# Kernel tuning notes

Hardware: AMD Instinct MI355X
Metric: run time of the kernel (lower is better)

## Reference

```python
import jax, jax.numpy as jnp
import numpy as np

B, H, S, D = 2, 16, 2048, 128


def setup_inputs() -> dict:
    key = jax.random.key(0)
    ks = jax.random.split(key, 11)
    s = 1.0 / np.sqrt(D)
    return {
        "query": jax.random.normal(ks[0], (B, H, S, D), dtype=jnp.float32),
        "key": jax.random.normal(ks[1], (B, H, S, D), dtype=jnp.float32),
        "value": jax.random.normal(ks[2], (B, H, S, D), dtype=jnp.float32),
        "Wq": jax.random.normal(ks[3], (D, D), dtype=jnp.float32) * s,
        "bq": jnp.zeros((D,), dtype=jnp.float32),
        "Wk": jax.random.normal(ks[4], (D, D), dtype=jnp.float32) * s,
        "bk": jnp.zeros((D,), dtype=jnp.float32),
        "Wv": jax.random.normal(ks[5], (D, D), dtype=jnp.float32) * s,
        "bv": jnp.zeros((D,), dtype=jnp.float32),
        "Wo": jax.random.normal(ks[6], (D, D), dtype=jnp.float32) * s,
        "bo": jnp.zeros((D,), dtype=jnp.float32),
    }


def reference(query, key, value, Wq, bq, Wk, bk, Wv, bv, Wo, bo):
    # Linear projections (torch Linear: x @ W^T + b) on last dim of [B,H,S,D]
    q = jnp.einsum("bhsd,ed->bhse", query, Wq) + bq
    k = jnp.einsum("bhsd,ed->bhse", key, Wk) + bk
    v = jnp.einsum("bhsd,ed->bhse", value, Wv) + bv
    scale = jnp.sqrt(jnp.asarray(D, dtype=q.dtype))
    q = q / scale
    qk = jnp.einsum("bhse,bhte->bhst", q, k)  # [B,H,S,S] scores
    attn = jax.nn.softmax(qk, axis=-1)
    # dropout_p = 0.0 -> identity
    out = jnp.einsum("bhst,bhtd->bhsd", attn, v)
    out = jnp.einsum("bhsd,ed->bhse", out, Wo) + bo
    return out
```

## Files before the change

### kernel.cpp

```cpp
#include <hip/hip_runtime.h>
#include <hip/hip_bf16.h>
#include <type_traits>
#include <math.h>

typedef __bf16 bf16x8 __attribute__((ext_vector_type(8)));
typedef float floatx4 __attribute__((ext_vector_type(4)));
typedef float floatx16 __attribute__((ext_vector_type(16)));

#define S_LEN 2048
#define D_DIM 128
#define NTOK (2 * 16 * 2048)
#define KVB 64
#define NKV (S_LEN / KVB)

template <typename TIN, typename TOUT>
__device__ __forceinline__ void proj_body4(
    const TIN* __restrict__ x, const float* __restrict__ W,
    const float* __restrict__ b, TOUT* __restrict__ y, float out_scale,
    int chunk0, __bf16 (*Wl)[128]) {
  const int tid = threadIdx.x;
  const int wave = tid >> 6, lane = tid & 63;
  const int g = lane >> 4, lr = lane & 15;

  for (int it = 0; it < 16; ++it) {
    int lin = it * 1024 + tid * 4;
    float4 w4 = *reinterpret_cast<const float4*>(W + lin);
    int r = lin >> 7, c = lin & 127;
    Wl[r][c]     = (__bf16)w4.x;
    Wl[r][c + 1] = (__bf16)w4.y;
    Wl[r][c + 2] = (__bf16)w4.z;
    Wl[r][c + 3] = (__bf16)w4.w;
  }
  __syncthreads();

  float be[8];
#pragma unroll
  for (int nt = 0; nt < 8; ++nt) be[nt] = b[nt * 16 + lr];

  for (int ch = 0; ch < 4; ++ch) {
    const int rbase = (chunk0 + ch) * 64;
    const int arow = rbase + wave * 16 + lr;

    floatx4 acc[8];
#pragma unroll
    for (int i = 0; i < 8; ++i) acc[i] = floatx4{0.f, 0.f, 0.f, 0.f};

#pragma unroll
    for (int kc = 0; kc < 4; ++kc) {
      bf16x8 af;
      const TIN* xp = x + (size_t)arow * D_DIM + kc * 32 + g * 8;
      if constexpr (std::is_same<TIN, float>::value) {
        float4 f0 = *reinterpret_cast<const float4*>(xp);
        float4 f1 = *reinterpret_cast<const float4*>(xp + 4);
        af[0] = (__bf16)f0.x; af[1] = (__bf16)f0.y;
        af[2] = (__bf16)f0.z; af[3] = (__bf16)f0.w;
        af[4] = (__bf16)f1.x; af[5] = (__bf16)f1.y;
        af[6] = (__bf16)f1.z; af[7] = (__bf16)f1.w;
      } else {
        af = *reinterpret_cast<const bf16x8*>(xp);
      }
#pragma unroll
      for (int nt = 0; nt < 8; ++nt) {
        bf16x8 wf = *reinterpret_cast<const bf16x8*>(&Wl[nt * 16 + lr][kc * 32 + g * 8]);
        acc[nt] = __builtin_amdgcn_mfma_f32_16x16x32_bf16(af, wf, acc[nt], 0, 0, 0);
      }
    }

#pragma unroll
    for (int nt = 0; nt < 8; ++nt) {
      int e = nt * 16 + lr;
#pragma unroll
      for (int j = 0; j < 4; ++j) {
        int row = rbase + wave * 16 + g * 4 + j;
        float val = (acc[nt][j] + be[nt]) * out_scale;
        y[(size_t)row * D_DIM + e] = (TOUT)val;
      }
    }
  }
}

__global__ __launch_bounds__(256) void qkv_proj_kernel(
    const float* __restrict__ xq, const float* __restrict__ xk,
    const float* __restrict__ xv, const float* __restrict__ Wq,
    const float* __restrict__ Wk, const float* __restrict__ Wv,
    const float* __restrict__ bq, const float* __restrict__ bk,
    const float* __restrict__ bv, __bf16* yq, __bf16* yk, __bf16* yv,
    float qscale) {
  __shared__ alignas(16) __bf16 Wl[128][128];
  const int which = blockIdx.y;
  const float* x = which == 0 ? xq : which == 1 ? xk : xv;
  const float* W = which == 0 ? Wq : which == 1 ? Wk : Wv;
  const float* b = which == 0 ? bq : which == 1 ? bk : bv;
  __bf16* y = which == 0 ? yq : which == 1 ? yk : yv;
  float sc = which == 0 ? qscale : 1.0f;
  proj_body4<float, __bf16>(x, W, b, y, sc, blockIdx.x * 4, Wl);
}

__global__ __launch_bounds__(256) void o_proj_kernel(
    const __bf16* __restrict__ x, const float* __restrict__ W,
    const float* __restrict__ b, float* __restrict__ y) {
  __shared__ alignas(16) __bf16 Wl[128][128];
  proj_body4<__bf16, float>(x, W, b, y, 1.0f, blockIdx.x * 4, Wl);
}

__device__ __forceinline__ unsigned swz(int row, unsigned byteoff) {
  return byteoff ^ (((unsigned)(row ^ (row >> 3)) & 7u) << 4);
}

__device__ __forceinline__ unsigned pack2(float lo, float hi) {
  union { __bf16 h[2]; unsigned u; } r;
  r.h[0] = (__bf16)lo; r.h[1] = (__bf16)hi;
  return r.u;
}

__global__ __launch_bounds__(256, 2) void attn_kernel(
    const __bf16* __restrict__ q, const __bf16* __restrict__ k,
    const __bf16* __restrict__ v, __bf16* __restrict__ o) {
  __shared__ alignas(16) unsigned char smem[65536];

  const int tid = threadIdx.x;
  const int wave = tid >> 6, lane = tid & 63;
  const int ql = lane & 31;
  const int h = lane >> 5;

  const int bh = blockIdx.x;
  const int qbase = blockIdx.y * 128;
  const __bf16* qp = q + (size_t)bh * S_LEN * D_DIM;
  const __bf16* kp = k + (size_t)bh * S_LEN * D_DIM;
  const __bf16* vp = v + (size_t)bh * S_LEN * D_DIM;
  __bf16* op = o + (size_t)bh * S_LEN * D_DIM;

  const int qrow = qbase + wave * 32 + ql;
  bf16x8 qf[8];
#pragma unroll
  for (int kc = 0; kc < 8; ++kc)
    qf[kc] = *reinterpret_cast<const bf16x8*>(
        qp + (size_t)qrow * D_DIM + kc * 16 + h * 8);

  floatx16 ot[4];
#pragma unroll
  for (int d = 0; d < 4; ++d)
#pragma unroll
    for (int r = 0; r < 16; ++r) ot[d][r] = 0.f;
  float m_r = -1e30f, l_r = 0.f;

  const int cc = tid & 15;
  const int pr4 = (tid >> 4) * 4;
  const int ce = cc * 8;

  unsigned Rk[4];
#pragma unroll
  for (int x = 0; x < 4; ++x)
    Rk[x] = (unsigned)(h * 1024) +
            (((unsigned)(ql * 16)) ^ ((unsigned)h << 4) ^ ((unsigned)x << 5));
  const unsigned Rv0 = 32768u + (unsigned)(h * 2048) +
                       (((unsigned)(ql * 16)) ^ (((unsigned)(ql >> 3)) << 4));
  const unsigned Rv1 = Rv0 ^ 64u;
  const unsigned kx = ((unsigned)(cc & 7)) << 4;
  unsigned Wk_[4];
#pragma unroll
  for (int j = 0; j < 4; ++j)
    Wk_[j] = ((unsigned)(cc * 1024 + (pr4 + j) * 16)) ^ kx;
  unsigned Wv_[8];
  {
    unsigned vbase = 32768u + (unsigned)((pr4 >> 3) * 2048 + ce * 16 + (pr4 & 7) * 2);
#pragma unroll
    for (int e = 0; e < 8; ++e)
      Wv_[e] = vbase | (((unsigned)e << 4) ^ kx);
  }

  {
    const __bf16* kr = kp + (size_t)pr4 * D_DIM + ce;
    const __bf16* vr = vp + (size_t)pr4 * D_DIM + ce;
    bf16x8 kR[4];
    union { bf16x8 v8; unsigned short s[8]; } vR[4];
#pragma unroll
    for (int j = 0; j < 4; ++j) {
      kR[j] = *reinterpret_cast<const bf16x8*>(kr + j * D_DIM);
      vR[j].v8 = *reinterpret_cast<const bf16x8*>(vr + j * D_DIM);
    }
#pragma unroll
    for (int j = 0; j < 4; ++j)
      *reinterpret_cast<bf16x8*>(smem + Wk_[j]) = kR[j];
#pragma unroll
    for (int e = 0; e < 8; ++e) {
      uint2 w;
      w.x = (unsigned)vR[0].s[e] | ((unsigned)vR[1].s[e] << 16);
      w.y = (unsigned)vR[2].s[e] | ((unsigned)vR[3].s[e] << 16);
      *reinterpret_cast<uint2*>(smem + Wv_[e]) = w;
    }
  }

  const __bf16* krp = kp + ((size_t)KVB + pr4) * D_DIM + ce;
  const __bf16* vrp = vp + ((size_t)KVB + pr4) * D_DIM + ce;

#pragma unroll 2
  for (int t = 0; t < NKV; ++t) {
    const unsigned cb = (unsigned)(t & 1) * 16384u;
    const bool hn = (t + 1 < NKV);

    __syncthreads();

    bf16x8 kR[4];
    union { bf16x8 v8; unsigned short s[8]; } vR[4];
    if (hn) {
#pragma unroll
      for (int j = 0; j < 4; ++j) {
        kR[j] = *reinterpret_cast<const bf16x8*>(krp + j * D_DIM);
        vR[j].v8 = *reinterpret_cast<const bf16x8*>(vrp + j * D_DIM);
      }
      krp += (size_t)KVB * D_DIM;
      vrp += (size_t)KVB * D_DIM;
    }

    floatx16 st[2];
#pragma unroll
    for (int kvh = 0; kvh < 2; ++kvh)
#pragma unroll
      for (int r = 0; r < 16; ++r) st[kvh][r] = 0.f;
    __builtin_amdgcn_s_setprio(1);
#pragma unroll
    for (int kc = 0; kc < 8; ++kc) {
      bf16x8 kf0 = *reinterpret_cast<const bf16x8*>(
          smem + cb + Rk[kc & 3] + (unsigned)(kc * 2048));
      bf16x8 kf1 = *reinterpret_cast<const bf16x8*>(
          smem + cb + Rk[kc & 3] + (unsigned)(kc * 2048 + 512));
      st[0] = __builtin_amdgcn_mfma_f32_32x32x16_bf16(kf0, qf[kc], st[0], 0, 0, 0);
      st[1] = __builtin_amdgcn_mfma_f32_32x32x16_bf16(kf1, qf[kc], st[1], 0, 0, 0);
    }
    __builtin_amdgcn_s_setprio(0);

    if (hn) {
      const unsigned nb = cb ^ 16384u;
#pragma unroll
      for (int j = 0; j < 4; ++j)
        *reinterpret_cast<bf16x8*>(smem + nb + Wk_[j]) = kR[j];
#pragma unroll
      for (int e = 0; e < 8; ++e) {
        uint2 w;
        w.x = (unsigned)vR[0].s[e] | ((unsigned)vR[1].s[e] << 16);
        w.y = (unsigned)vR[2].s[e] | ((unsigned)vR[3].s[e] << 16);
        *reinterpret_cast<uint2*>(smem + nb + Wv_[e]) = w;
      }
    }

    float t8[8];
#pragma unroll
    for (int i = 0; i < 8; ++i)
      t8[i] = fmaxf(fmaxf(st[0][i], st[0][i + 8]), fmaxf(st[1][i], st[1][i + 8]));
    float pmax = fmaxf(fmaxf(fmaxf(t8[0], t8[4]), fmaxf(t8[1], t8[5])),
                       fmaxf(fmaxf(t8[2], t8[6]), fmaxf(t8[3], t8[7])));
    pmax = fmaxf(pmax, __shfl_xor(pmax, 32));
    if (!__all(pmax - m_r <= 8.0f)) {
      float mnew = fmaxf(m_r, pmax);
      float sc_f = __builtin_amdgcn_exp2f(m_r - mnew);
      m_r = mnew;
      l_r *= sc_f;
#pragma unroll
      for (int d = 0; d < 4; ++d)
#pragma unroll
        for (int r = 0; r < 16; ++r) ot[d][r] *= sc_f;
    }
#pragma unroll
    for (int kvh = 0; kvh < 2; ++kvh)
#pragma unroll
      for (int r = 0; r < 16; ++r)
        st[kvh][r] = __builtin_amdgcn_exp2f(st[kvh][r] - m_r);
    float s8[8];
#pragma unroll
    for (int i = 0; i < 8; ++i)
      s8[i] = (st[0][i] + st[0][i + 8]) + (st[1][i] + st[1][i + 8]);
    float psum = ((s8[0] + s8[4]) + (s8[1] + s8[5])) +
                 ((s8[2] + s8[6]) + (s8[3] + s8[7]));
    psum += __shfl_xor(psum, 32);
    l_r += psum;

#pragma unroll
    for (int ks = 0; ks < 4; ++ks) {
      const int kvh = ks >> 1;
      const int r2a = (2 * ks) & 3;
      const int r2b = r2a + 1;
      unsigned ua0 = pack2(st[kvh][r2a * 4 + 0], st[kvh][r2a * 4 + 1]);
      unsigned ua1 = pack2(st[kvh][r2a * 4 + 2], st[kvh][r2a * 4 + 3]);
      unsigned ub0 = pack2(st[kvh][r2b * 4 + 0], st[kvh][r2b * 4 + 1]);
      unsigned ub1 = pack2(st[kvh][r2b * 4 + 2], st[kvh][r2b * 4 + 3]);
      union { unsigned u[4]; bf16x8 v8; } pw;
#if __has_builtin(__builtin_amdgcn_permlane32_swap)
      {
        auto r0 = __builtin_amdgcn_permlane32_swap(ua0, ub0, false, false);
        auto r1 = __builtin_amdgcn_permlane32_swap(ua1, ub1, false, false);
        pw.u[0] = r0[0];
        pw.u[1] = r1[0];
        pw.u[2] = r0[1];
        pw.u[3] = r1[1];
      }
#else
      {
        unsigned a0x = __shfl_xor(ua0, 32), a1x = __shfl_xor(ua1, 32);
        unsigned b0x = __shfl_xor(ub0, 32), b1x = __shfl_xor(ub1, 32);
        pw.u[0] = h ? b0x : ua0;
        pw.u[1] = h ? b1x : ua1;
        pw.u[2] = h ? ub0 : a0x;
        pw.u[3] = h ? ub1 : a1x;
      }
#endif
      __builtin_amdgcn_s_setprio(1);
#pragma unroll
      for (int db = 0; db < 4; ++db) {
        const unsigned base = (db & 1) ? Rv1 : Rv0;
        bf16x8 vf = *reinterpret_cast<const bf16x8*>(
            smem + cb + base + (unsigned)(ks * 4096 + db * 512));
        ot[db] = __builtin_amdgcn_mfma_f32_32x32x16_bf16(vf, pw.v8, ot[db], 0, 0, 0);
      }
      __builtin_amdgcn_s_setprio(0);
    }
  }

  __syncthreads();
  const float inv_l = 1.0f / l_r;
  const int qloc = wave * 32 + ql;
#pragma unroll
  for (int db = 0; db < 4; ++db)
#pragma unroll
    for (int r = 0; r < 16; ++r) {
      int d = db * 32 + (r & 3) + 8 * (r >> 2) + 4 * h;
      *reinterpret_cast<__bf16*>(smem + swz(qloc, qloc * 256u + d * 2u)) =
          (__bf16)(ot[db][r] * inv_l);
    }
  __syncthreads();
#pragma unroll
  for (int it = 0; it < 8; ++it) {
    int r = tid >> 1;
    int c = (tid & 1) * 64 + it * 8;
    bf16x8 val = *reinterpret_cast<const bf16x8*>(smem + swz(r, r * 256u + c * 2u));
    *reinterpret_cast<bf16x8*>(op + (size_t)(qbase + r) * D_DIM + c) = val;
  }
}

extern "C" void kernel_launch(void* const* d_in, const int* in_sizes, int n_in,
                              void* d_out, int out_size, void* d_ws, size_t ws_size,
                              hipStream_t stream) {
  const float* query = (const float*)d_in[0];
  const float* key_  = (const float*)d_in[1];
  const float* value = (const float*)d_in[2];
  const float* Wq = (const float*)d_in[3];
  const float* bq = (const float*)d_in[4];
  const float* Wk = (const float*)d_in[5];
  const float* bk = (const float*)d_in[6];
  const float* Wv = (const float*)d_in[7];
  const float* bv = (const float*)d_in[8];
  const float* Wo = (const float*)d_in[9];
  const float* bo = (const float*)d_in[10];

  __bf16* vws = (__bf16*)d_ws;
  __bf16* aws = vws + (size_t)NTOK * D_DIM;
  __bf16* qws = (__bf16*)d_out;
  __bf16* kws = qws + (size_t)NTOK * D_DIM;

  const float qscale = 0.1275174490036f;

  qkv_proj_kernel<<<dim3(NTOK / 256, 3), dim3(256), 0, stream>>>(
      query, key_, value, Wq, Wk, Wv, bq, bk, bv, qws, kws, vws, qscale);

  attn_kernel<<<dim3(32, 16), dim3(256), 0, stream>>>(qws, kws, vws, aws);

  o_proj_kernel<<<NTOK / 256, dim3(256), 0, stream>>>(aws, Wo, bo, (float*)d_out);
}
```

Measured before the change: 132.0 us.

## Fuse output projection into attention kernel epilogue

Adds an attention kernel whose epilogue stages the normalized attention tile and a bf16 copy of Wo in shared memory, then applies the output projection with MFMA and writes fp32 results directly. This removes the separate o_proj launch and the global round trip of the bf16 attention output. When the workspace is large enough, Q/K/V move into the workspace so they no longer alias the output buffer. Each attention block now converts all of Wo itself, which adds redundant loads and a longer tail per block. The old three-kernel path is kept as a fallback for small workspaces.

New measurement: 123.5 us, median of 2. -6.5%, faster.

```diff
diff --git a/kernel.cpp b/kernel.cpp
--- a/kernel.cpp
+++ b/kernel.cpp
@@ -113,9 +113,10 @@
   return r.u;
 }
 
-__global__ __launch_bounds__(256, 2) void attn_kernel(
+__global__ __launch_bounds__(256, 2) void attn_fused_kernel(
     const __bf16* __restrict__ q, const __bf16* __restrict__ k,
-    const __bf16* __restrict__ v, __bf16* __restrict__ o) {
+    const __bf16* __restrict__ v, const float* __restrict__ Wo,
+    const float* __restrict__ bo, float* __restrict__ out) {
   __shared__ alignas(16) unsigned char smem[65536];
 
   const int tid = threadIdx.x;
@@ -128,7 +129,6 @@
   const __bf16* qp = q + (size_t)bh * S_LEN * D_DIM;
   const __bf16* kp = k + (size_t)bh * S_LEN * D_DIM;
   const __bf16* vp = v + (size_t)bh * S_LEN * D_DIM;
-  __bf16* op = o + (size_t)bh * S_LEN * D_DIM;
 
   const int qrow = qbase + wave * 32 + ql;
   bf16x8 qf[8];
@@ -317,6 +317,269 @@
   }
 
   __syncthreads();
+
+  {
+    const float inv_l = 1.0f / l_r;
+    const int qloc = wave * 32 + ql;
+#pragma unroll
+    for (int db = 0; db < 4; ++db)
+#pragma unroll
+      for (int r = 0; r < 16; ++r) {
+        int d = db * 32 + (r & 3) + 8 * (r >> 2) + 4 * h;
+        *reinterpret_cast<__bf16*>(smem + swz(qloc, qloc * 256u + d * 2u)) =
+            (__bf16)(ot[db][r] * inv_l);
+      }
+  }
+  for (int it = 0; it < 16; ++it) {
+    int lin = it * 1024 + tid * 4;
+    float4 w4 = *reinterpret_cast<const float4*>(Wo + lin);
+    int r = lin >> 7, c = lin & 127;
+    unsigned off = 32768u + swz(r, (unsigned)(r * 256 + c * 2));
+    __bf16 b4[4] = {(__bf16)w4.x, (__bf16)w4.y, (__bf16)w4.z, (__bf16)w4.w};
+    *reinterpret_cast<uint2*>(smem + off) = *reinterpret_cast<uint2*>(b4);
+  }
+  __syncthreads();
+
+  const int g4 = lane >> 4;
+  const int lr = lane & 15;
+  float be[8];
+#pragma unroll
+  for (int nt = 0; nt < 8; ++nt) be[nt] = bo[nt * 16 + lr];
+
+#pragma unroll
+  for (int rt = 0; rt < 2; ++rt) {
+    const int arow = wave * 32 + rt * 16 + lr;
+    floatx4 acc[8];
+#pragma unroll
+    for (int i = 0; i < 8; ++i) acc[i] = floatx4{0.f, 0.f, 0.f, 0.f};
+#pragma unroll
+    for (int kc = 0; kc < 4; ++kc) {
+      bf16x8 af = *reinterpret_cast<const bf16x8*>(
+          smem + swz(arow, (unsigned)(arow * 256 + (kc * 32 + g4 * 8) * 2)));
+#pragma unroll
+      for (int nt = 0; nt < 8; ++nt) {
+        int wrow = nt * 16 + lr;
+        bf16x8 wf = *reinterpret_cast<const bf16x8*>(
+            smem + 32768u + swz(wrow, (unsigned)(wrow * 256 + (kc * 32 + g4 * 8) * 2)));
+        acc[nt] = __builtin_amdgcn_mfma_f32_16x16x32_bf16(af, wf, acc[nt], 0, 0, 0);
+      }
+    }
+#pragma unroll
+    for (int nt = 0; nt < 8; ++nt) {
+      int e = nt * 16 + lr;
+#pragma unroll
+      for (int j = 0; j < 4; ++j) {
+        int row = qbase + wave * 32 + rt * 16 + g4 * 4 + j;
+        out[((size_t)bh * S_LEN + row) * D_DIM + e] = acc[nt][j] + be[nt];
+      }
+    }
+  }
+}
+
+__global__ __launch_bounds__(256, 2) void attn_kernel(
+    const __bf16* __restrict__ q, const __bf16* __restrict__ k,
+    const __bf16* __restrict__ v, __bf16* __restrict__ o) {
+  __shared__ alignas(16) unsigned char smem[65536];
+
+  const int tid = threadIdx.x;
+  const int wave = tid >> 6, lane = tid & 63;
+  const int ql = lane & 31;
+  const int h = lane >> 5;
+
+  const int bh = blockIdx.x;
+  const int qbase = blockIdx.y * 128;
+  const __bf16* qp = q + (size_t)bh * S_LEN * D_DIM;
+  const __bf16* kp = k + (size_t)bh * S_LEN * D_DIM;
+  const __bf16* vp = v + (size_t)bh * S_LEN * D_DIM;
+  __bf16* op = o + (size_t)bh * S_LEN * D_DIM;
+
+  const int qrow = qbase + wave * 32 + ql;
+  bf16x8 qf[8];
+#pragma unroll
+  for (int kc = 0; kc < 8; ++kc)
+    qf[kc] = *reinterpret_cast<const bf16x8*>(
+        qp + (size_t)qrow * D_DIM + kc * 16 + h * 8);
+
+  floatx16 ot[4];
+#pragma unroll
+  for (int d = 0; d < 4; ++d)
+#pragma unroll
+    for (int r = 0; r < 16; ++r) ot[d][r] = 0.f;
+  float m_r = -1e30f, l_r = 0.f;
+
+  const int cc = tid & 15;
+  const int pr4 = (tid >> 4) * 4;
+  const int ce = cc * 8;
+
+  unsigned Rk[4];
+#pragma unroll
+  for (int x = 0; x < 4; ++x)
+    Rk[x] = (unsigned)(h * 1024) +
+            (((unsigned)(ql * 16)) ^ ((unsigned)h << 4) ^ ((unsigned)x << 5));
+  const unsigned Rv0 = 32768u + (unsigned)(h * 2048) +
+                       (((unsigned)(ql * 16)) ^ (((unsigned)(ql >> 3)) << 4));
+  const unsigned Rv1 = Rv0 ^ 64u;
+  const unsigned kx = ((unsigned)(cc & 7)) << 4;
+  unsigned Wk_[4];
+#pragma unroll
+  for (int j = 0; j < 4; ++j)
+    Wk_[j] = ((unsigned)(cc * 1024 + (pr4 + j) * 16)) ^ kx;
+  unsigned Wv_[8];
+  {
+    unsigned vbase = 32768u + (unsigned)((pr4 >> 3) * 2048 + ce * 16 + (pr4 & 7) * 2);
+#pragma unroll
+    for (int e = 0; e < 8; ++e)
+      Wv_[e] = vbase | (((unsigned)e << 4) ^ kx);
+  }
+
+  {
+    const __bf16* kr = kp + (size_t)pr4 * D_DIM + ce;
+    const __bf16* vr = vp + (size_t)pr4 * D_DIM + ce;
+    bf16x8 kR[4];
+    union { bf16x8 v8; unsigned short s[8]; } vR[4];
+#pragma unroll
+    for (int j = 0; j < 4; ++j) {
+      kR[j] = *reinterpret_cast<const bf16x8*>(kr + j * D_DIM);
+      vR[j].v8 = *reinterpret_cast<const bf16x8*>(vr + j * D_DIM);
+    }
+#pragma unroll
+    for (int j = 0; j < 4; ++j)
+      *reinterpret_cast<bf16x8*>(smem + Wk_[j]) = kR[j];
+#pragma unroll
+    for (int e = 0; e < 8; ++e) {
+      uint2 w;
+      w.x = (unsigned)vR[0].s[e] | ((unsigned)vR[1].s[e] << 16);
+      w.y = (unsigned)vR[2].s[e] | ((unsigned)vR[3].s[e] << 16);
+      *reinterpret_cast<uint2*>(smem + Wv_[e]) = w;
+    }
+  }
+
+  const __bf16* krp = kp + ((size_t)KVB + pr4) * D_DIM + ce;
+  const __bf16* vrp = vp + ((size_t)KVB + pr4) * D_DIM + ce;
+
+#pragma unroll 2
+  for (int t = 0; t < NKV; ++t) {
+    const unsigned cb = (unsigned)(t & 1) * 16384u;
+    const bool hn = (t + 1 < NKV);
+
+    __syncthreads();
+
+    bf16x8 kR[4];
+    union { bf16x8 v8; unsigned short s[8]; } vR[4];
+    if (hn) {
+#pragma unroll
+      for (int j = 0; j < 4; ++j) {
+        kR[j] = *reinterpret_cast<const bf16x8*>(krp + j * D_DIM);
+        vR[j].v8 = *reinterpret_cast<const bf16x8*>(vrp + j * D_DIM);
+      }
+      krp += (size_t)KVB * D_DIM;
+      vrp += (size_t)KVB * D_DIM;
+    }
+
+    floatx16 st[2];
+#pragma unroll
+    for (int kvh = 0; kvh < 2; ++kvh)
+#pragma unroll
+      for (int r = 0; r < 16; ++r) st[kvh][r] = 0.f;
+    __builtin_amdgcn_s_setprio(1);
+#pragma unroll
+    for (int kc = 0; kc < 8; ++kc) {
+      bf16x8 kf0 = *reinterpret_cast<const bf16x8*>(
+          smem + cb + Rk[kc & 3] + (unsigned)(kc * 2048));
+      bf16x8 kf1 = *reinterpret_cast<const bf16x8*>(
+          smem + cb + Rk[kc & 3] + (unsigned)(kc * 2048 + 512));
+      st[0] = __builtin_amdgcn_mfma_f32_32x32x16_bf16(kf0, qf[kc], st[0], 0, 0, 0);
+      st[1] = __builtin_amdgcn_mfma_f32_32x32x16_bf16(kf1, qf[kc], st[1], 0, 0, 0);
+    }
+    __builtin_amdgcn_s_setprio(0);
+
+    if (hn) {
+      const unsigned nb = cb ^ 16384u;
+#pragma unroll
+      for (int j = 0; j < 4; ++j)
+        *reinterpret_cast<bf16x8*>(smem + nb + Wk_[j]) = kR[j];
+#pragma unroll
+      for (int e = 0; e < 8; ++e) {
+        uint2 w;
+        w.x = (unsigned)vR[0].s[e] | ((unsigned)vR[1].s[e] << 16);
+        w.y = (unsigned)vR[2].s[e] | ((unsigned)vR[3].s[e] << 16);
+        *reinterpret_cast<uint2*>(smem + nb + Wv_[e]) = w;
+      }
+    }
+
+    float t8[8];
+#pragma unroll
+    for (int i = 0; i < 8; ++i)
+      t8[i] = fmaxf(fmaxf(st[0][i], st[0][i + 8]), fmaxf(st[1][i], st[1][i + 8]));
+    float pmax = fmaxf(fmaxf(fmaxf(t8[0], t8[4]), fmaxf(t8[1], t8[5])),
+                       fmaxf(fmaxf(t8[2], t8[6]), fmaxf(t8[3], t8[7])));
+    pmax = fmaxf(pmax, __shfl_xor(pmax, 32));
+    if (!__all(pmax - m_r <= 8.0f)) {
+      float mnew = fmaxf(m_r, pmax);
+      float sc_f = __builtin_amdgcn_exp2f(m_r - mnew);
+      m_r = mnew;
+      l_r *= sc_f;
+#pragma unroll
+      for (int d = 0; d < 4; ++d)
+#pragma unroll
+        for (int r = 0; r < 16; ++r) ot[d][r] *= sc_f;
+    }
+#pragma unroll
+    for (int kvh = 0; kvh < 2; ++kvh)
+#pragma unroll
+      for (int r = 0; r < 16; ++r)
+        st[kvh][r] = __builtin_amdgcn_exp2f(st[kvh][r] - m_r);
+    float s8[8];
+#pragma unroll
+    for (int i = 0; i < 8; ++i)
+      s8[i] = (st[0][i] + st[0][i + 8]) + (st[1][i] + st[1][i + 8]);
+    float psum = ((s8[0] + s8[4]) + (s8[1] + s8[5])) +
+                 ((s8[2] + s8[6]) + (s8[3] + s8[7]));
+    psum += __shfl_xor(psum, 32);
+    l_r += psum;
+
+#pragma unroll
+    for (int ks = 0; ks < 4; ++ks) {
+      const int kvh = ks >> 1;
+      const int r2a = (2 * ks) & 3;
+      const int r2b = r2a + 1;
+      unsigned ua0 = pack2(st[kvh][r2a * 4 + 0], st[kvh][r2a * 4 + 1]);
+      unsigned ua1 = pack2(st[kvh][r2a * 4 + 2], st[kvh][r2a * 4 + 3]);
+      unsigned ub0 = pack2(st[kvh][r2b * 4 + 0], st[kvh][r2b * 4 + 1]);
+      unsigned ub1 = pack2(st[kvh][r2b * 4 + 2], st[kvh][r2b * 4 + 3]);
+      union { unsigned u[4]; bf16x8 v8; } pw;
+#if __has_builtin(__builtin_amdgcn_permlane32_swap)
+      {
+        auto r0 = __builtin_amdgcn_permlane32_swap(ua0, ub0, false, false);
+        auto r1 = __builtin_amdgcn_permlane32_swap(ua1, ub1, false, false);
+        pw.u[0] = r0[0];
+        pw.u[1] = r1[0];
+        pw.u[2] = r0[1];
+        pw.u[3] = r1[1];
+      }
+#else
+      {
+        unsigned a0x = __shfl_xor(ua0, 32), a1x = __shfl_xor(ua1, 32);
+        unsigned b0x = __shfl_xor(ub0, 32), b1x = __shfl_xor(ub1, 32);
+        pw.u[0] = h ? b0x : ua0;
+        pw.u[1] = h ? b1x : ua1;
+        pw.u[2] = h ? ub0 : a0x;
+        pw.u[3] = h ? ub1 : a1x;
+      }
+#endif
+      __builtin_amdgcn_s_setprio(1);
+#pragma unroll
+      for (int db = 0; db < 4; ++db) {
+        const unsigned base = (db & 1) ? Rv1 : Rv0;
+        bf16x8 vf = *reinterpret_cast<const bf16x8*>(
+            smem + cb + base + (unsigned)(ks * 4096 + db * 512));
+        ot[db] = __builtin_amdgcn_mfma_f32_32x32x16_bf16(vf, pw.v8, ot[db], 0, 0, 0);
+      }
+      __builtin_amdgcn_s_setprio(0);
+    }
+  }
+
+  __syncthreads();
   const float inv_l = 1.0f / l_r;
   const int qloc = wave * 32 + ql;
 #pragma unroll
@@ -352,17 +615,31 @@
   const float* Wo = (const float*)d_in[9];
   const float* bo = (const float*)d_in[10];
 
-  __bf16* vws = (__bf16*)d_ws;
-  __bf16* aws = vws + (size_t)NTOK * D_DIM;
-  __bf16* qws = (__bf16*)d_out;
-  __bf16* kws = qws + (size_t)NTOK * D_DIM;
-
+  const size_t nelem = (size_t)NTOK * D_DIM;
   const float qscale = 0.1275174490036f;
-
-  qkv_proj_kernel<<<dim3(NTOK / 256, 3), dim3(256), 0, stream>>>(
-      query, key_, value, Wq, Wk, Wv, bq, bk, bv, qws, kws, vws, qscale);
-
-  attn_kernel<<<dim3(32, 16), dim3(256), 0, stream>>>(qws, kws, vws, aws);
-
-  o_proj_kernel<<<NTOK / 256, dim3(256), 0, stream>>>(aws, Wo, bo, (float*)d_out);
-}
+  dim3 blk(256);
+
+  if (ws_size >= 3 * nelem * sizeof(__bf16)) {
+    __bf16* vws = (__bf16*)d_ws;
+    __bf16* qws = vws + nelem;
+    __bf16* kws = qws + nelem;
+
+    qkv_proj_kernel<<<dim3(NTOK / 256, 3), blk, 0, stream>>>(
+        query, key_, value, Wq, Wk, Wv, bq, bk, bv, qws, kws, vws, qscale);
+
+    attn_fused_kernel<<<dim3(32, 16), blk, 0, stream>>>(
+        qws, kws, vws, Wo, bo, (float*)d_out);
+  } else {
+    __bf16* vws = (__bf16*)d_ws;
+    __bf16* aws = vws + nelem;
+    __bf16* qws = (__bf16*)d_out;
+    __bf16* kws = qws + nelem;
+
+    qkv_proj_kernel<<<dim3(NTOK / 256, 3), blk, 0, stream>>>(
+        query, key_, value, Wq, Wk, Wv, bq, bk, bv, qws, kws, vws, qscale);
+
+    attn_kernel<<<dim3(32, 16), blk, 0, stream>>>(qws, kws, vws, aws);
+
+    o_proj_kernel<<<NTOK / 256, blk, 0, stream>>>(aws, Wo, bo, (float*)d_out);
+  }
+}
```
